# Optimization experiments

Measured on AMD Instinct MI355X. Metric: run time of the kernel, lower is better.

Reference implementation:

```python
import jax, jax.numpy as jnp
import numpy as np

DIM = 768
HEADS = 12
HEAD_DIM = DIM // HEADS
WS = 32                      # window_size (Wh == Ww)
N = WS * WS + 1              # tokens = patches + CLS
B = 8
NUM_REL = (2 * WS - 1) * (2 * WS - 1) + 3


def _rel_pos_index():
    # Mirrors the torch buffer construction (meshgrid indexing='ij').
    coords = np.stack(np.meshgrid(np.arange(WS), np.arange(WS), indexing='ij')).reshape(2, -1)
    rel = (coords[:, :, None] - coords[:, None, :]).transpose(1, 2, 0)  # [M, M, 2]
    rel[..., 0] += WS - 1
    rel[..., 1] += WS - 1
    rel[..., 0] *= 2 * WS - 1
    idx = np.zeros((N, N), dtype=np.int32)
    idx[1:, 1:] = rel.sum(-1)
    idx[0, :] = NUM_REL - 3
    idx[:, 0] = NUM_REL - 2
    idx[0, 0] = NUM_REL - 1
    return idx


def setup_inputs() -> dict:
    key = jax.random.key(0)
    ks = jax.random.split(key, 4)
    s = DIM ** -0.5
    return {
        "x": jax.random.normal(ks[0], (B, N, DIM), dtype=jnp.float32),
        "qkv_w": jax.random.normal(ks[1], (3 * DIM, DIM), dtype=jnp.float32) * s,
        "q_bias": jnp.zeros((DIM,), dtype=jnp.float32),
        "v_bias": jnp.zeros((DIM,), dtype=jnp.float32),
        "rpb_table": jax.random.normal(ks[2], (NUM_REL, HEADS), dtype=jnp.float32) * 0.02,
        "proj_w": jax.random.normal(ks[3], (DIM, DIM), dtype=jnp.float32) * s,
        "proj_b": jnp.zeros((DIM,), dtype=jnp.float32),
        "rel_pos_index": jnp.asarray(_rel_pos_index()),
    }


def reference(x, qkv_w, q_bias, v_bias, rpb_table, proj_w, proj_b, rel_pos_index):
    Bx, Nx, C = x.shape
    scale = HEAD_DIM ** -0.5
    # qkv bias = [q_bias, zeros, v_bias] (k has no bias)
    qkv_bias = jnp.concatenate([q_bias, jnp.zeros_like(v_bias), v_bias])
    qkv = x @ qkv_w.T + qkv_bias                           # [B, N, 3*C]
    qkv = qkv.reshape(Bx, Nx, 3, HEADS, HEAD_DIM).transpose(2, 0, 3, 1, 4)
    q, k, v = qkv[0] * scale, qkv[1], qkv[2]               # [B, H, N, d]
    attn = jnp.einsum('bhqd,bhkd->bhqk', q, k)             # [B, H, N, N]
    rpb = rpb_table[rel_pos_index]                         # [N, N, H] gather
    attn = attn + rpb.transpose(2, 0, 1)[None]             # broadcast over batch
    attn = jax.nn.softmax(attn, axis=-1)
    out = jnp.einsum('bhqk,bhkd->bhqd', attn, v)           # [B, H, N, d]
    out = out.transpose(0, 2, 1, 3).reshape(Bx, Nx, -1)    # [B, N, C]
    return out @ proj_w.T + proj_b
```

## Files before the change

kernel.cpp:

```cpp
#include <hip/hip_runtime.h>

typedef _Float16 f16;
typedef __attribute__((ext_vector_type(4))) _Float16 f16x4;
typedef __attribute__((ext_vector_type(8))) _Float16 f16x8;
typedef __attribute__((ext_vector_type(4))) float f32x4;

#define BATCH 8
#define NTOK 1025
#define DIM 768
#define HEADS 12
#define HD 64
#define MTOT (BATCH * NTOK)
#define MPAD 8320
#define NQP2 1152
#define NKP 1088
#define NUMREL 3972

#define DMA_FENCE asm volatile("s_waitcnt vmcnt(0)" ::: "memory")

__device__ __forceinline__ int imin(int a, int b) { return a < b ? a : b; }

__device__ __forceinline__ void gl_lds16(const f16* g, f16* l) {
  __builtin_amdgcn_global_load_lds(
      (const __attribute__((address_space(1))) unsigned int*)g,
      (__attribute__((address_space(3))) unsigned int*)l, 16, 0, 0);
}

__global__ __launch_bounds__(256) void cast3(const float* __restrict__ s0,
                                             f16* __restrict__ d0, int n0,
                                             const float* __restrict__ s1,
                                             f16* __restrict__ d1, int n1,
                                             const float* __restrict__ s2,
                                             f16* __restrict__ d2, int n2) {
  const float* s = (blockIdx.y == 0) ? s0 : (blockIdx.y == 1) ? s1 : s2;
  f16* d = (blockIdx.y == 0) ? d0 : (blockIdx.y == 1) ? d1 : d2;
  int n = (blockIdx.y == 0) ? n0 : (blockIdx.y == 1) ? n1 : n2;
  for (size_t i = ((size_t)blockIdx.x * 256 + threadIdx.x) * 8; i < (size_t)n;
       i += (size_t)gridDim.x * 256 * 8) {
    float4 a = *(const float4*)(s + i);
    float4 b = *(const float4*)(s + i + 4);
    f16x8 r;
    r[0] = (f16)a.x; r[1] = (f16)a.y; r[2] = (f16)a.z; r[3] = (f16)a.w;
    r[4] = (f16)b.x; r[5] = (f16)b.y; r[6] = (f16)b.z; r[7] = (f16)b.w;
    *(f16x8*)(d + i) = r;
  }
}

__device__ __forceinline__ float rpb_bias(const float* __restrict__ rpb, int qg,
                                          int kg, int h) {
  int idx;
  if (kg == 0) {
    idx = (qg == 0) ? (NUMREL - 1) : (NUMREL - 2);
  } else if (qg == 0) {
    idx = NUMREL - 3;
  } else {
    int qq = imin(qg, 1024) - 1, kk = imin(kg, 1024) - 1;
    int di = (qq >> 5) - (kk >> 5);
    int dj = (qq & 31) - (kk & 31);
    idx = (di + 31) * 63 + (dj + 31);
  }
  return rpb[idx * HEADS + h];
}

__global__ __launch_bounds__(256) void bias_pre(const float* __restrict__ rpb,
                                                f16* __restrict__ tbl) {
  const int kt = blockIdx.x / 17;
  const int qb17 = blockIdx.x % 17;
  const int h = blockIdx.y;
  const int tid = threadIdx.x;
  const int q = qb17 * 64 + (tid >> 2);
  const int lg = tid & 3;
  f16 vals[16];
#pragma unroll
  for (int c = 0; c < 4; c++)
#pragma unroll
    for (int r = 0; r < 4; r++) {
      int kv = kt * 64 + c * 16 + lg * 4 + r;
      float v = (kv >= NTOK) ? -30000.f : rpb_bias(rpb, q, kv, h);
      vals[c * 4 + r] = (f16)v;
    }
  size_t off = ((((size_t)h * 17 + kt) * NKP + q) * 4 + lg) * 16;
  *(f16x8*)(tbl + off) = *(const f16x8*)(&vals[0]);
  *(f16x8*)(tbl + off + 8) = *(const f16x8*)(&vals[8]);
}

__global__ __launch_bounds__(512) void qkv_gemm(
    const f16* __restrict__ Ah, const f16* __restrict__ Bh,
    const float* __restrict__ q_bias, const float* __restrict__ v_bias,
    f16* __restrict__ qb, f16* __restrict__ kb, f16* __restrict__ vtb) {
  __shared__ f16 As[128][64];
  __shared__ f16 Bs[256][64];
  const int tid = threadIdx.x;
  const int lane = tid & 63, w = tid >> 6;
  const int wm = w >> 2, wn = w & 3;
  const int lr = lane & 15, lg = lane >> 4;
  const int tN = blockIdx.x;
  const int tM = blockIdx.y;
  const int r8 = lane >> 3;
  const int swch = (lane & 7) ^ r8;
  const int lr7 = lr & 7;

  const f16* Ab = Ah + ((size_t)tM * 128 + r8) * DIM + swch * 8;
  const f16* Bb = Bh + ((size_t)tN * 256 + r8) * DIM + swch * 8;

  f32x4 acc[4][4] = {};

  for (int kt = 0; kt < 12; kt++) {
#pragma unroll
    for (int pp = 0; pp < 2; pp++) {
      int rowb = w * 16 + pp * 8;
      gl_lds16(Ab + (size_t)rowb * DIM + kt * 64, &As[rowb][0]);
    }
#pragma unroll
    for (int pp = 0; pp < 4; pp++) {
      int rowb = w * 32 + pp * 8;
      gl_lds16(Bb + (size_t)rowb * DIM + kt * 64, &Bs[rowb][0]);
    }
    DMA_FENCE;
    __syncthreads();
#pragma unroll
    for (int ks = 0; ks < 2; ks++) {
      f16x8 af[4], bf[4];
      int rc = ((ks * 4 + lg) ^ lr7) * 8;
#pragma unroll
      for (int i = 0; i < 4; i++) {
        af[i] = *(const f16x8*)(&As[wm * 64 + i * 16 + lr][rc]);
        bf[i] = *(const f16x8*)(&Bs[wn * 64 + i * 16 + lr][rc]);
      }
#pragma unroll
      for (int mi = 0; mi < 4; mi++)
#pragma unroll
        for (int ni = 0; ni < 4; ni++)
          acc[mi][ni] = __builtin_amdgcn_mfma_f32_16x16x32_f16(
              af[mi], bf[ni], acc[mi][ni], 0, 0, 0);
    }
    __syncthreads();
  }

  const int which = tN / 3;
  const int nb = tN % 3;
#pragma unroll
  for (int mi = 0; mi < 4; mi++) {
#pragma unroll
    for (int ni = 0; ni < 4; ni++) {
      int ncol = nb * 256 + wn * 64 + ni * 16 + lr;
      int h = ncol >> 6, dd = ncol & 63;
      float bias = 0.f;
      if (which == 0) bias = q_bias[ncol];
      if (which == 2) bias = v_bias[ncol];
#pragma unroll
      for (int r = 0; r < 4; r++) {
        int m = tM * 128 + wm * 64 + mi * 16 + lg * 4 + r;
        if (m >= MTOT) continue;
        int b = m / NTOK;
        int t = m - b * NTOK;
        int bh = b * HEADS + h;
        float v = acc[mi][ni][r] + bias;
        if (which == 0)
          qb[((size_t)bh * NQP2 + t) * HD + dd] = (f16)(v * 0.125f);
        else if (which == 1)
          kb[((size_t)bh * NKP + t) * HD + dd] = (f16)v;
        else
          vtb[((size_t)bh * HD + dd) * NKP + t] = (f16)v;
      }
    }
  }
}

__global__ __launch_bounds__(256) void attn_kernel(
    const f16* __restrict__ qb, const f16* __restrict__ kb,
    const f16* __restrict__ vtb, const f16* __restrict__ tbl,
    f16* __restrict__ ob) {
  __shared__ f16 Ks[2][64][64];
  __shared__ f16 Vs[2][64][64];
  __shared__ f16 Plds[4][16][72];
  const int tid = threadIdx.x;
  const int lane = tid & 63, w = tid >> 6;
  const int lr = lane & 15, lg = lane >> 4;
  const int b = blockIdx.x & 7;
  const int t9 = blockIdx.x >> 3;
  const int qblk = t9 % 9;
  const int h = t9 / 9;
  const int bh = b * HEADS + h;
  const int q0 = qblk * 128 + w * 32;

  const f16* kbase = kb + (size_t)bh * NKP * HD;
  const f16* vbase = vtb + (size_t)bh * HD * NKP;

  const int srow8 = lane >> 3;
  const int swch = (lane & 7) ^ srow8;

#pragma unroll
  for (int pp = 0; pp < 2; pp++) {
    int p = w * 2 + pp;
    int row = p * 8 + srow8;
    gl_lds16(kbase + (size_t)row * HD + swch * 8, &Ks[0][p * 8][0]);
    gl_lds16(vbase + (size_t)row * NKP + swch * 8, &Vs[0][p * 8][0]);
  }

  f16x8 aq[2][2];
#pragma unroll
  for (int g = 0; g < 2; g++) {
    const f16* qp = qb + ((size_t)bh * NQP2 + q0 + g * 16 + lr) * HD + lg * 8;
    aq[g][0] = *(const f16x8*)(qp);
    aq[g][1] = *(const f16x8*)(qp + 32);
  }

  const f16* bp[2];
#pragma unroll
  for (int g = 0; g < 2; g++) {
    int qt = imin(q0 + g * 16 + lr, NKP - 1);
    bp[g] = tbl + (((size_t)h * 17 * NKP + qt) * 4 + lg) * 16;
  }
  f16x8 bb[2][2];
#pragma unroll
  for (int g = 0; g < 2; g++) {
    bb[g][0] = *(const f16x8*)(bp[g]);
    bb[g][1] = *(const f16x8*)(bp[g] + 8);
  }

  float lsum[2] = {0.f, 0.f};
  f32x4 oacc[2][4] = {};
  const int sw8 = lr & 7;
  const size_t ktstride = (size_t)NKP * 64;

  for (int kt = 0; kt < 17; kt++) {
    const int bi = kt & 1;
    DMA_FENCE;
    __syncthreads();
    if (kt + 1 < 17) {
#pragma unroll
      for (int pp = 0; pp < 2; pp++) {
        int p = w * 2 + pp;
        int row = p * 8 + srow8;
        gl_lds16(kbase + (size_t)((kt + 1) * 64 + row) * HD + swch * 8,
                 &Ks[bi ^ 1][p * 8][0]);
        gl_lds16(vbase + (size_t)row * NKP + (kt + 1) * 64 + swch * 8,
                 &Vs[bi ^ 1][p * 8][0]);
      }
    }
    f16x8 nb[2][2] = {};
    if (kt + 1 < 17) {
#pragma unroll
      for (int g = 0; g < 2; g++) {
        const f16* p8 = bp[g] + (size_t)(kt + 1) * ktstride;
        nb[g][0] = *(const f16x8*)(p8);
        nb[g][1] = *(const f16x8*)(p8 + 8);
      }
    }
    f32x4 s[2][4];
#pragma unroll
    for (int g = 0; g < 2; g++)
#pragma unroll
      for (int c = 0; c < 4; c++) {
        const f16* src = (const f16*)&bb[g][c >> 1];
#pragma unroll
        for (int r = 0; r < 4; r++) s[g][c][r] = (float)src[(c & 1) * 4 + r];
      }
#pragma unroll
    for (int c = 0; c < 4; c++) {
      f16x8 kf0 = *(const f16x8*)(&Ks[bi][c * 16 + lr][(lg ^ sw8) * 8]);
      f16x8 kf1 = *(const f16x8*)(&Ks[bi][c * 16 + lr][((lg + 4) ^ sw8) * 8]);
      s[0][c] = __builtin_amdgcn_mfma_f32_16x16x32_f16(kf0, aq[0][0], s[0][c], 0, 0, 0);
      s[0][c] = __builtin_amdgcn_mfma_f32_16x16x32_f16(kf1, aq[0][1], s[0][c], 0, 0, 0);
      s[1][c] = __builtin_amdgcn_mfma_f32_16x16x32_f16(kf0, aq[1][0], s[1][c], 0, 0, 0);
      s[1][c] = __builtin_amdgcn_mfma_f32_16x16x32_f16(kf1, aq[1][1], s[1][c], 0, 0, 0);
    }
#pragma unroll
    for (int g = 0; g < 2; g++)
#pragma unroll
      for (int c = 0; c < 4; c++)
#pragma unroll
        for (int r = 0; r < 4; r++) {
          float p = __expf(s[g][c][r]);
          s[g][c][r] = p;
          lsum[g] += p;
        }
    f16x8 ap[2][2];
#pragma unroll
    for (int g = 0; g < 2; g++) {
#pragma unroll
      for (int c = 0; c < 4; c++) {
        f16x4 pk;
        pk[0] = (f16)s[g][c][0];
        pk[1] = (f16)s[g][c][1];
        pk[2] = (f16)s[g][c][2];
        pk[3] = (f16)s[g][c][3];
        *(f16x4*)(&Plds[w][lr][c * 16 + lg * 4]) = pk;
      }
      ap[g][0] = *(const f16x8*)(&Plds[w][lr][lg * 8]);
      ap[g][1] = *(const f16x8*)(&Plds[w][lr][32 + lg * 8]);
    }
#pragma unroll
    for (int dblk = 0; dblk < 4; dblk++) {
      f16x8 vf0 = *(const f16x8*)(&Vs[bi][dblk * 16 + lr][(lg ^ sw8) * 8]);
      f16x8 vf1 = *(const f16x8*)(&Vs[bi][dblk * 16 + lr][((lg + 4) ^ sw8) * 8]);
      oacc[0][dblk] = __builtin_amdgcn_mfma_f32_16x16x32_f16(ap[0][0], vf0, oacc[0][dblk], 0, 0, 0);
      oacc[0][dblk] = __builtin_amdgcn_mfma_f32_16x16x32_f16(ap[0][1], vf1, oacc[0][dblk], 0, 0, 0);
      oacc[1][dblk] = __builtin_amdgcn_mfma_f32_16x16x32_f16(ap[1][0], vf0, oacc[1][dblk], 0, 0, 0);
      oacc[1][dblk] = __builtin_amdgcn_mfma_f32_16x16x32_f16(ap[1][1], vf1, oacc[1][dblk], 0, 0, 0);
    }
#pragma unroll
    for (int g = 0; g < 2; g++) {
      bb[g][0] = nb[g][0];
      bb[g][1] = nb[g][1];
    }
  }
#pragma unroll
  for (int g = 0; g < 2; g++) {
    float ls = lsum[g];
    ls += __shfl_xor(ls, 16);
    ls += __shfl_xor(ls, 32);
    float inv[4];
#pragma unroll
    for (int r = 0; r < 4; r++) inv[r] = 1.f / __shfl(ls, lg * 4 + r);
#pragma unroll
    for (int dblk = 0; dblk < 4; dblk++)
#pragma unroll
      for (int r = 0; r < 4; r++) {
        int qg = q0 + g * 16 + lg * 4 + r;
        if (qg >= NTOK) continue;
        float v = oacc[g][dblk][r] * inv[r];
        ob[((size_t)(b * NTOK + qg)) * DIM + h * HD + dblk * 16 + lr] = (f16)v;
      }
  }
}

__global__ __launch_bounds__(512) void proj_gemm(const f16* __restrict__ Ah,
                                                 const f16* __restrict__ Bh,
                                                 const float* __restrict__ pb,
                                                 float* __restrict__ out) {
  __shared__ f16 As[128][64];
  __shared__ f16 Bs[256][64];
  const int tid = threadIdx.x;
  const int lane = tid & 63, w = tid >> 6;
  const int wm = w >> 2, wn = w & 3;
  const int lr = lane & 15, lg = lane >> 4;
  const int tN = blockIdx.x;
  const int tM = blockIdx.y;
  const int r8 = lane >> 3;
  const int swch = (lane & 7) ^ r8;
  const int lr7 = lr & 7;

  const f16* Ab = Ah + ((size_t)tM * 128 + r8) * DIM + swch * 8;
  const f16* Bb = Bh + ((size_t)tN * 256 + r8) * DIM + swch * 8;

  f32x4 acc[4][4] = {};

  for (int kt = 0; kt < 12; kt++) {
#pragma unroll
    for (int pp = 0; pp < 2; pp++) {
      int rowb = w * 16 + pp * 8;
      gl_lds16(Ab + (size_t)rowb * DIM + kt * 64, &As[rowb][0]);
    }
#pragma unroll
    for (int pp = 0; pp < 4; pp++) {
      int rowb = w * 32 + pp * 8;
      gl_lds16(Bb + (size_t)rowb * DIM + kt * 64, &Bs[rowb][0]);
    }
    DMA_FENCE;
    __syncthreads();
#pragma unroll
    for (int ks = 0; ks < 2; ks++) {
      f16x8 af[4], bf[4];
      int rc = ((ks * 4 + lg) ^ lr7) * 8;
#pragma unroll
      for (int i = 0; i < 4; i++) {
        af[i] = *(const f16x8*)(&As[wm * 64 + i * 16 + lr][rc]);
        bf[i] = *(const f16x8*)(&Bs[wn * 64 + i * 16 + lr][rc]);
      }
#pragma unroll
      for (int mi = 0; mi < 4; mi++)
#pragma unroll
        for (int ni = 0; ni < 4; ni++)
          acc[mi][ni] = __builtin_amdgcn_mfma_f32_16x16x32_f16(
              af[mi], bf[ni], acc[mi][ni], 0, 0, 0);
    }
    __syncthreads();
  }

#pragma unroll
  for (int mi = 0; mi < 4; mi++) {
#pragma unroll
    for (int ni = 0; ni < 4; ni++) {
      int n = tN * 256 + wn * 64 + ni * 16 + lr;
      float bias = pb[n];
#pragma unroll
      for (int r = 0; r < 4; r++) {
        int m = tM * 128 + wm * 64 + mi * 16 + lg * 4 + r;
        if (m >= MTOT) continue;
        out[(size_t)m * DIM + n] = acc[mi][ni][r] + bias;
      }
    }
  }
}

extern "C" void kernel_launch(void* const* d_in, const int* in_sizes, int n_in,
                              void* d_out, int out_size, void* d_ws,
                              size_t ws_size, hipStream_t stream) {
  const float* x = (const float*)d_in[0];
  const float* qkv_w = (const float*)d_in[1];
  const float* q_bias = (const float*)d_in[2];
  const float* v_bias = (const float*)d_in[3];
  const float* rpb = (const float*)d_in[4];
  const float* proj_w = (const float*)d_in[5];
  const float* proj_b = (const float*)d_in[6];
  float* out = (float*)d_out;

  f16* xh = (f16*)d_ws;
  f16* wh = xh + (size_t)MPAD * DIM;
  f16* pwh = wh + (size_t)3 * DIM * DIM;
  f16* qb = pwh + (size_t)DIM * DIM;
  f16* kb = qb + (size_t)BATCH * HEADS * NQP2 * HD;
  f16* vtb = kb + (size_t)BATCH * HEADS * NKP * HD;
  f16* ob = vtb + (size_t)BATCH * HEADS * NKP * HD;
  f16* tbl = ob + (size_t)MPAD * DIM;

  cast3<<<dim3(1024, 3), 256, 0, stream>>>(
      x, xh, MTOT * DIM, qkv_w, wh, 3 * DIM * DIM, proj_w, pwh, DIM * DIM);
  bias_pre<<<dim3(17 * 17, HEADS), 256, 0, stream>>>(rpb, tbl);
  qkv_gemm<<<dim3(9, 65), 512, 0, stream>>>(xh, wh, q_bias, v_bias, qb, kb,
                                            vtb);
  attn_kernel<<<dim3(BATCH * HEADS * 9), 256, 0, stream>>>(qb, kb, vtb, tbl,
                                                           ob);
  proj_gemm<<<dim3(3, 65), 512, 0, stream>>>(ob, pwh, proj_b, out);
}
```

Baseline: 277.4 us.

## Pair two query blocks per 512-thread attention workgroup to share K/V tiles

The attention kernel now launches 512-thread workgroups in which two groups of four waves each handle a different 128-query block of the same batch and head. They share one double-buffered K/V tile stream in LDS, with each wave loading a single 8-row slice. This halves global K/V traffic per query and reduces the block count. In exchange, the nine query blocks are rounded up to ten, so one block per head does padded, wasted work. There are also fewer, larger workgroups, which changes occupancy and scheduling balance.

```diff
diff --git a/kernel.cpp b/kernel.cpp
--- a/kernel.cpp
+++ b/kernel.cpp
@@ -167,22 +167,23 @@
   }
 }
 
-__global__ __launch_bounds__(256) void attn_kernel(
+__global__ __launch_bounds__(512) void attn_kernel(
     const f16* __restrict__ qb, const f16* __restrict__ kb,
     const f16* __restrict__ vtb, const f16* __restrict__ tbl,
     f16* __restrict__ ob) {
   __shared__ f16 Ks[2][64][64];
   __shared__ f16 Vs[2][64][64];
-  __shared__ f16 Plds[4][16][72];
+  __shared__ f16 Plds[8][16][72];
   const int tid = threadIdx.x;
   const int lane = tid & 63, w = tid >> 6;
   const int lr = lane & 15, lg = lane >> 4;
   const int b = blockIdx.x & 7;
-  const int t9 = blockIdx.x >> 3;
-  const int qblk = t9 % 9;
-  const int h = t9 / 9;
+  const int t5 = blockIdx.x >> 3;
+  const int qpair = t5 % 5;
+  const int h = t5 / 5;
+  const int qblk = qpair * 2 + (w >> 2);
   const int bh = b * HEADS + h;
-  const int q0 = qblk * 128 + w * 32;
+  const int q0 = qblk * 128 + (w & 3) * 32;
 
   const f16* kbase = kb + (size_t)bh * NKP * HD;
   const f16* vbase = vtb + (size_t)bh * HD * NKP;
@@ -190,12 +191,10 @@
   const int srow8 = lane >> 3;
   const int swch = (lane & 7) ^ srow8;
 
-#pragma unroll
-  for (int pp = 0; pp < 2; pp++) {
-    int p = w * 2 + pp;
-    int row = p * 8 + srow8;
-    gl_lds16(kbase + (size_t)row * HD + swch * 8, &Ks[0][p * 8][0]);
-    gl_lds16(vbase + (size_t)row * NKP + swch * 8, &Vs[0][p * 8][0]);
+  {
+    int row = w * 8 + srow8;
+    gl_lds16(kbase + (size_t)row * HD + swch * 8, &Ks[0][w * 8][0]);
+    gl_lds16(vbase + (size_t)row * NKP + swch * 8, &Vs[0][w * 8][0]);
   }
 
   f16x8 aq[2][2];
@@ -229,15 +228,11 @@
     DMA_FENCE;
     __syncthreads();
     if (kt + 1 < 17) {
-#pragma unroll
-      for (int pp = 0; pp < 2; pp++) {
-        int p = w * 2 + pp;
-        int row = p * 8 + srow8;
-        gl_lds16(kbase + (size_t)((kt + 1) * 64 + row) * HD + swch * 8,
-                 &Ks[bi ^ 1][p * 8][0]);
-        gl_lds16(vbase + (size_t)row * NKP + (kt + 1) * 64 + swch * 8,
-                 &Vs[bi ^ 1][p * 8][0]);
-      }
+      int row = w * 8 + srow8;
+      gl_lds16(kbase + (size_t)((kt + 1) * 64 + row) * HD + swch * 8,
+               &Ks[bi ^ 1][w * 8][0]);
+      gl_lds16(vbase + (size_t)row * NKP + (kt + 1) * 64 + swch * 8,
+               &Vs[bi ^ 1][w * 8][0]);
     }
     f16x8 nb[2][2] = {};
     if (kt + 1 < 17) {
@@ -421,7 +416,7 @@
   bias_pre<<<dim3(17 * 17, HEADS), 256, 0, stream>>>(rpb, tbl);
   qkv_gemm<<<dim3(9, 65), 512, 0, stream>>>(xh, wh, q_bias, v_bias, qb, kb,
                                             vtb);
-  attn_kernel<<<dim3(BATCH * HEADS * 9), 256, 0, stream>>>(qb, kb, vtb, tbl,
+  attn_kernel<<<dim3(BATCH * 5 * HEADS), 512, 0, stream>>>(qb, kb, vtb, tbl,
                                                            ob);
   proj_gemm<<<dim3(3, 65), 512, 0, stream>>>(ob, pwh, proj_b, out);
 }
```

Result: no change. 274.7 us (-1.0%).
